# Performance work log

Measured on AMD Instinct MI355X. Metric: run time of the kernel, lower is better.

The kernel has to match this reference:

```python
import jax, jax.numpy as jnp
import numpy as np
from jax import lax

SAMPLING_FRACTION = 0.5
BIG = 1e8  # initial 'infinite' distance, matches torch's 1e8


def _farthest_point_sample(points, init_idx, n_sample):
    """points: (B,N,C) float; init_idx: (B,) int. Returns (B, n_sample) int32 indices."""
    B, N, C = points.shape
    batch = jnp.arange(B)

    def step(carry, _):
        distances, farthest = carry            # (B,N), (B,)
        centroid = points[batch, farthest]     # (B,C)
        d = jnp.sum((points - centroid[:, None, :]) ** 2, axis=-1)  # (B,N) squared euclid
        distances = jnp.minimum(distances, d)
        new_farthest = jnp.argmax(distances, axis=-1)
        return (distances, new_farthest), farthest  # record index BEFORE update (matches torch)

    init = (jnp.full((B, N), BIG, dtype=points.dtype), init_idx.astype(jnp.int32))
    _, centroids = lax.scan(step, init, None, length=n_sample)
    return centroids.T  # (B, n_sample)


def _index_points(x, idx):
    # x: (B, N, ...) ; idx: (B, M) -> (B, M, ...)
    return jnp.take_along_axis(x, idx.reshape(idx.shape + (1,) * (x.ndim - 2)), axis=1) if x.ndim > 2 else jnp.take_along_axis(x, idx, axis=1)


def setup_inputs() -> dict:
    key = jax.random.key(0)
    k1, k2, k3 = jax.random.split(key, 3)
    B, N, C, D = 16, 8192, 3, 256
    coords = jax.random.normal(k1, (B, N, C), dtype=jnp.float32)
    values = jax.random.normal(k2, (B, N, D), dtype=jnp.float32)
    mask = jnp.ones((B, N), dtype=jnp.float32)
    init_idx = jax.random.randint(k3, (B,), 0, N)
    return {"coords": coords, "values": values, "mask": mask, "init_idx": init_idx}


def reference(coords, values, mask, init_idx):
    B, N, C = coords.shape
    n_sample = int(round(N * SAMPLING_FRACTION))
    idx = _farthest_point_sample(coords, init_idx, n_sample)  # (B, n_sample)
    query_coords = _index_points(coords, idx)  # (B, M, C)
    query_values = _index_points(values, idx)  # (B, M, D)
    query_mask = _index_points(mask, idx)      # (B, M)
    return (query_coords, query_values, query_mask)
```

## Files before the change

### kernel.cpp

```cpp
#include <hip/hip_runtime.h>

#define FPS_N   8192
#define FPS_T   1024
#define FPS_W   (FPS_T / 64)
#define FPS_PPT (FPS_N / FPS_T)

__device__ __forceinline__ float mul_rn(float a, float b) {
    float r; asm("v_mul_f32 %0, %1, %2" : "=v"(r) : "v"(a), "v"(b)); return r;
}

template<int CTRL>
__device__ __forceinline__ float dpp_max_step(float x) {
    int s = __builtin_amdgcn_update_dpp(0, __float_as_int(x), CTRL, 0xf, 0xf, true);
    return fmaxf(x, __int_as_float(s));
}

__device__ __forceinline__ float wave_max_nn(float x) {
    x = dpp_max_step<0x111>(x);
    x = dpp_max_step<0x112>(x);
    x = dpp_max_step<0x114>(x);
    x = dpp_max_step<0x118>(x);
    x = dpp_max_step<0x142>(x);
    x = dpp_max_step<0x143>(x);
    return __int_as_float(__builtin_amdgcn_readlane(__float_as_int(x), 63));
}

__global__ __launch_bounds__(FPS_T) void fps_kernel(
    const float* __restrict__ coords,
    const int*   __restrict__ init_idx,
    int*         __restrict__ out_idx,
    int M)
{
    __shared__ float sx[FPS_N], sy[FPS_N], sz[FPS_N];
    __shared__ float swd[2][FPS_W];
    __shared__ int   swi[2][FPS_W];

    const int b    = blockIdx.x;
    const int tid  = threadIdx.x;
    const int lane = tid & 63;
    const float* cb = coords + (size_t)b * FPS_N * 3;

    float f[24];
    const float4* cb4 = reinterpret_cast<const float4*>(cb);
    #pragma unroll
    for (int i = 0; i < 6; ++i) {
        float4 v = cb4[tid * 6 + i];
        f[i * 4 + 0] = v.x; f[i * 4 + 1] = v.y;
        f[i * 4 + 2] = v.z; f[i * 4 + 3] = v.w;
    }

    float px[FPS_PPT], py[FPS_PPT], pz[FPS_PPT], dist[FPS_PPT];
    const int base = tid * FPS_PPT;
    #pragma unroll
    for (int k = 0; k < FPS_PPT; ++k) {
        px[k] = f[3 * k + 0];
        py[k] = f[3 * k + 1];
        pz[k] = f[3 * k + 2];
        sx[base + k] = px[k];
        sy[base + k] = py[k];
        sz[base + k] = pz[k];
        dist[k] = 1e8f;
    }
    __syncthreads();

    int far = init_idx[b];

    for (int s = 0; s < M; ++s) {
        if (tid == 0) out_idx[b * M + s] = far;

        const float cx = sx[far], cy = sy[far], cz = sz[far];

        float m = 0.0f;
        #pragma unroll
        for (int k = 0; k < FPS_PPT; ++k) {
            float dx = px[k] - cx;
            float dy = py[k] - cy;
            float dz = pz[k] - cz;
            float d  = __builtin_fmaf(dz, dz,
                         __builtin_fmaf(dy, dy, mul_rn(dx, dx)));
            float nd = fminf(dist[k], d);
            dist[k]  = nd;
            m = fmaxf(m, nd);
        }
        int myidx = base;
        #pragma unroll
        for (int k = FPS_PPT - 1; k >= 0; --k)
            myidx = (dist[k] == m) ? base + k : myidx;

        float wm = wave_max_nn(m);
        unsigned long long ball = __ballot(m == wm);
        int fl   = (int)__builtin_ctzll(ball);
        int widx = __builtin_amdgcn_readlane(myidx, fl);

        const int par = s & 1;
        if (lane == 0) {
            swd[par][tid >> 6] = wm;
            swi[par][tid >> 6] = widx;
        }
        __syncthreads();

        float wv  = swd[par][lane & (FPS_W - 1)];
        int   wxi = swi[par][lane & (FPS_W - 1)];
        float gm  = wave_max_nn(wv);
        unsigned long long b2 = __ballot(wv == gm);
        int f2 = (int)__builtin_ctzll(b2);
        far = __builtin_amdgcn_readlane(wxi, f2);
    }
}

__global__ void gather_kernel(
    const float* __restrict__ coords,
    const float* __restrict__ values,
    const float* __restrict__ mask,
    const int*   __restrict__ idx,
    float* __restrict__ out_coords,
    float* __restrict__ out_values,
    float* __restrict__ out_mask,
    int N, int M, int D)
{
    const int bm = blockIdx.x;
    const int b  = bm / M;
    const int m  = bm - b * M;
    const int j  = idx[bm];
    const int l  = threadIdx.x;

    const float4* src = reinterpret_cast<const float4*>(values + ((size_t)b * N + j) * D);
    float4*       dst = reinterpret_cast<float4*>(out_values + ((size_t)b * M + m) * D);
    dst[l] = src[l];

    if (l < 3) {
        out_coords[((size_t)b * M + m) * 3 + l] = coords[((size_t)b * N + j) * 3 + l];
    } else if (l == 3) {
        out_mask[(size_t)b * M + m] = mask[(size_t)b * N + j];
    }
}

extern "C" void kernel_launch(void* const* d_in, const int* in_sizes, int n_in,
                              void* d_out, int out_size, void* d_ws, size_t ws_size,
                              hipStream_t stream)
{
    const float* coords   = (const float*)d_in[0];
    const float* values   = (const float*)d_in[1];
    const float* mask     = (const float*)d_in[2];
    const int*   init_idx = (const int*)d_in[3];

    const int B = in_sizes[3];
    const int N = in_sizes[2] / B;
    const int D = in_sizes[1] / (B * N);
    const int M = N / 2;

    float* out_coords = (float*)d_out;
    float* out_values = out_coords + (size_t)B * M * 3;
    float* out_mask   = out_values + (size_t)B * M * D;

    int* idx = (int*)d_ws;

    fps_kernel<<<B, FPS_T, 0, stream>>>(coords, init_idx, idx, M);
    gather_kernel<<<B * M, D / 4, 0, stream>>>(coords, values, mask, idx,
                                               out_coords, out_values, out_mask,
                                               N, M, D);
}
```

Baseline: 3.857 ms.

## Halve FPS block size, use packed f32 math, and broadcast centroid coords via LDS

Drops the FPS block from 1024 to 512 threads, giving each thread 16 points processed as packed pairs with v_pk_add/mul/fma_f32. Each wave leader now stores its candidate's coordinates next to the index, so the next centroid comes from readlanes instead of a dependent LDS load after the reduction. The cross-wave reduction shrinks to 8 waves with a 3-step DPP max. The goal is to shorten the serial per-iteration critical path (barrier, reduction and centroid fetch), at the cost of more registers and more serial work per thread.

```diff
diff --git a/kernel.cpp b/kernel.cpp
--- a/kernel.cpp
+++ b/kernel.cpp
@@ -1,12 +1,21 @@
 #include <hip/hip_runtime.h>
 
 #define FPS_N   8192
-#define FPS_T   1024
+#define FPS_T   512
 #define FPS_W   (FPS_T / 64)
 #define FPS_PPT (FPS_N / FPS_T)
+#define FPS_PR  (FPS_PPT / 2)
 
-__device__ __forceinline__ float mul_rn(float a, float b) {
-    float r; asm("v_mul_f32 %0, %1, %2" : "=v"(r) : "v"(a), "v"(b)); return r;
+typedef float v2f __attribute__((ext_vector_type(2)));
+
+__device__ __forceinline__ v2f pk_add(v2f a, v2f b) {
+    v2f r; asm("v_pk_add_f32 %0, %1, %2" : "=v"(r) : "v"(a), "v"(b)); return r;
+}
+__device__ __forceinline__ v2f pk_mul(v2f a, v2f b) {
+    v2f r; asm("v_pk_mul_f32 %0, %1, %2" : "=v"(r) : "v"(a), "v"(b)); return r;
+}
+__device__ __forceinline__ v2f pk_fma(v2f a, v2f b, v2f c) {
+    v2f r; asm("v_pk_fma_f32 %0, %1, %2, %3" : "=v"(r) : "v"(a), "v"(b), "v"(c)); return r;
 }
 
 template<int CTRL>
@@ -25,6 +34,10 @@
     return __int_as_float(__builtin_amdgcn_readlane(__float_as_int(x), 63));
 }
 
+__device__ __forceinline__ float readlane_f(float x, int l) {
+    return __int_as_float(__builtin_amdgcn_readlane(__float_as_int(x), l));
+}
+
 __global__ __launch_bounds__(FPS_T) void fps_kernel(
     const float* __restrict__ coords,
     const int*   __restrict__ init_idx,
@@ -34,58 +47,68 @@
     __shared__ float sx[FPS_N], sy[FPS_N], sz[FPS_N];
     __shared__ float swd[2][FPS_W];
     __shared__ int   swi[2][FPS_W];
+    __shared__ float scx[2][FPS_W], scy[2][FPS_W], scz[2][FPS_W];
 
     const int b    = blockIdx.x;
     const int tid  = threadIdx.x;
     const int lane = tid & 63;
+    const int wv   = tid >> 6;
     const float* cb = coords + (size_t)b * FPS_N * 3;
 
-    float f[24];
+    float f[48];
     const float4* cb4 = reinterpret_cast<const float4*>(cb);
     #pragma unroll
-    for (int i = 0; i < 6; ++i) {
-        float4 v = cb4[tid * 6 + i];
+    for (int i = 0; i < 12; ++i) {
+        float4 v = cb4[tid * 12 + i];
         f[i * 4 + 0] = v.x; f[i * 4 + 1] = v.y;
         f[i * 4 + 2] = v.z; f[i * 4 + 3] = v.w;
     }
 
-    float px[FPS_PPT], py[FPS_PPT], pz[FPS_PPT], dist[FPS_PPT];
+    v2f px[FPS_PR], py[FPS_PR], pz[FPS_PR], dist[FPS_PR];
     const int base = tid * FPS_PPT;
     #pragma unroll
     for (int k = 0; k < FPS_PPT; ++k) {
-        px[k] = f[3 * k + 0];
-        py[k] = f[3 * k + 1];
-        pz[k] = f[3 * k + 2];
-        sx[base + k] = px[k];
-        sy[base + k] = py[k];
-        sz[base + k] = pz[k];
-        dist[k] = 1e8f;
+        sx[base + k] = f[3 * k + 0];
+        sy[base + k] = f[3 * k + 1];
+        sz[base + k] = f[3 * k + 2];
+    }
+    #pragma unroll
+    for (int j = 0; j < FPS_PR; ++j) {
+        px[j] = v2f{f[6 * j + 0], f[6 * j + 3]};
+        py[j] = v2f{f[6 * j + 1], f[6 * j + 4]};
+        pz[j] = v2f{f[6 * j + 2], f[6 * j + 5]};
+        dist[j] = v2f{1e8f, 1e8f};
     }
     __syncthreads();
 
     int far = init_idx[b];
+    float cx = sx[far], cy = sy[far], cz = sz[far];
 
     for (int s = 0; s < M; ++s) {
         if (tid == 0) out_idx[b * M + s] = far;
 
-        const float cx = sx[far], cy = sy[far], cz = sz[far];
-
+        const v2f ncx = v2f{-cx, -cx};
+        const v2f ncy = v2f{-cy, -cy};
+        const v2f ncz = v2f{-cz, -cz};
         float m = 0.0f;
         #pragma unroll
-        for (int k = 0; k < FPS_PPT; ++k) {
-            float dx = px[k] - cx;
-            float dy = py[k] - cy;
-            float dz = pz[k] - cz;
-            float d  = __builtin_fmaf(dz, dz,
-                         __builtin_fmaf(dy, dy, mul_rn(dx, dx)));
-            float nd = fminf(dist[k], d);
-            dist[k]  = nd;
-            m = fmaxf(m, nd);
+        for (int j = 0; j < FPS_PR; ++j) {
+            v2f dx2 = pk_add(px[j], ncx);
+            v2f dy2 = pk_add(py[j], ncy);
+            v2f dz2 = pk_add(pz[j], ncz);
+            v2f d2  = pk_fma(dz2, dz2, pk_fma(dy2, dy2, pk_mul(dx2, dx2)));
+            v2f nd;
+            nd.x = fminf(dist[j].x, d2.x);
+            nd.y = fminf(dist[j].y, d2.y);
+            dist[j] = nd;
+            m = fmaxf(m, fmaxf(nd.x, nd.y));
         }
         int myidx = base;
         #pragma unroll
-        for (int k = FPS_PPT - 1; k >= 0; --k)
-            myidx = (dist[k] == m) ? base + k : myidx;
+        for (int j = FPS_PR - 1; j >= 0; --j) {
+            myidx = (dist[j].y == m) ? base + 2 * j + 1 : myidx;
+            myidx = (dist[j].x == m) ? base + 2 * j     : myidx;
+        }
 
         float wm = wave_max_nn(m);
         unsigned long long ball = __ballot(m == wm);
@@ -94,17 +117,29 @@
 
         const int par = s & 1;
         if (lane == 0) {
-            swd[par][tid >> 6] = wm;
-            swi[par][tid >> 6] = widx;
+            float wcx = sx[widx], wcy = sy[widx], wcz = sz[widx];
+            swd[par][wv] = wm;  swi[par][wv] = widx;
+            scx[par][wv] = wcx; scy[par][wv] = wcy; scz[par][wv] = wcz;
         }
         __syncthreads();
 
-        float wv  = swd[par][lane & (FPS_W - 1)];
-        int   wxi = swi[par][lane & (FPS_W - 1)];
-        float gm  = wave_max_nn(wv);
-        unsigned long long b2 = __ballot(wv == gm);
-        int f2 = (int)__builtin_ctzll(b2);
-        far = __builtin_amdgcn_readlane(wxi, f2);
+        float dval = 0.0f, cxl = 0.0f, cyl = 0.0f, czl = 0.0f;
+        int   idxl = 0;
+        if (lane < FPS_W) {
+            dval = swd[par][lane]; idxl = swi[par][lane];
+            cxl  = scx[par][lane]; cyl = scy[par][lane]; czl = scz[par][lane];
+        }
+        float g = dval;
+        g = dpp_max_step<0x111>(g);
+        g = dpp_max_step<0x112>(g);
+        g = dpp_max_step<0x114>(g);
+        float gm = readlane_f(g, 7);
+        unsigned long long b2 = __ballot(lane < FPS_W && dval == gm);
+        int w2 = (int)__builtin_ctzll(b2);
+        far = __builtin_amdgcn_readlane(idxl, w2);
+        cx  = readlane_f(cxl, w2);
+        cy  = readlane_f(cyl, w2);
+        cz  = readlane_f(czl, w2);
     }
 }
 
```

Measured after the change: 3.792 ms. No clear change (-1.7%).
